# Kernel optimization log

Hardware: AMD Instinct MI355X
Metric: run time of the kernel (lower is better)

## Reference

```python
import jax, jax.numpy as jnp
import numpy as np

I, H, O = 3, 16, 5
B, S = 4096, 512


def setup_inputs() -> dict:
    key = jax.random.key(0)
    ks = jax.random.split(key, 4)
    scale = 0.1  # xavier gain=0.1 ballpark; exact init irrelevant for correctness baseline
    return {
        "x": jax.random.normal(ks[0], (B, S, I), dtype=jnp.float32),
        "W_ih": jax.random.normal(ks[1], (4 * H, I), dtype=jnp.float32) * scale,
        "W_hh": jax.random.normal(ks[2], (4 * H, H), dtype=jnp.float32) * scale,
        "b_ih": jnp.zeros((4 * H,), dtype=jnp.float32),
        "b_hh": jnp.zeros((4 * H,), dtype=jnp.float32),
        "W_lin": jax.random.normal(ks[3], (O, H), dtype=jnp.float32) * scale,
        "b_lin": jnp.zeros((O,), dtype=jnp.float32),
    }


def _lstm(x, W_ih, W_hh, b_ih, b_hh):
    # Precompute input contribution for all timesteps: [B, S, 4H]
    xg = jnp.einsum('bsi,gi->bsg', x, W_ih) + b_ih + b_hh
    xg = jnp.swapaxes(xg, 0, 1)  # [S, B, 4H] for scan
    h0 = jnp.zeros((x.shape[0], H), dtype=x.dtype)
    c0 = jnp.zeros_like(h0)

    def step(carry, xt):
        h, c = carry
        gates = xt + h @ W_hh.T  # [B, 4H]
        i, f, g, o = jnp.split(gates, 4, axis=-1)  # PyTorch gate order i,f,g,o
        i = jax.nn.sigmoid(i)
        f = jax.nn.sigmoid(f)
        g = jnp.tanh(g)
        o = jax.nn.sigmoid(o)
        c = f * c + i * g
        h = o * jnp.tanh(c)
        return (h, c), h

    _, hs = jax.lax.scan(step, (h0, c0), xg)
    return jnp.swapaxes(hs, 0, 1)  # [B, S, H]


def reference(x, W_ih, W_hh, b_ih, b_hh, W_lin, b_lin):
    out1 = _lstm(x, W_ih, W_hh, b_ih, b_hh)            # [B, S, H]
    out = jnp.einsum('bsh,oh->bso', out1, W_lin) + b_lin  # [B, S, O]
    return jnp.clip(out, -10.0, 10.0)
```

## Files before the change

kernel.cpp:

```cpp
#include <hip/hip_runtime.h>


#define TS 512
#define LOG2E 1.44269504088896340736f

typedef float f32x2 __attribute__((ext_vector_type(2)));

#define BCAST(K) hbr[K] = __int_as_float( \
    __builtin_amdgcn_update_dpp(0, hvi, 0x150 + (K), 0xf, 0xf, true))
#define BCAST8() \
  BCAST(0); BCAST(1); BCAST(2); BCAST(3); BCAST(4); BCAST(5); BCAST(6); BCAST(7)

static __device__ __forceinline__ float swz16(float v) {
  return __int_as_float(__builtin_amdgcn_ds_swizzle(__float_as_int(v), 0x401F));
}

__global__ __launch_bounds__(256)
__attribute__((amdgpu_waves_per_eu(2)))
void lstm_enc_kernel(const float* __restrict__ x,
                     const float* __restrict__ W_ih,
                     const float* __restrict__ W_hh,
                     const float* __restrict__ b_ih,
                     const float* __restrict__ b_hh,
                     const float* __restrict__ W_lin,
                     const float* __restrict__ b_lin,
                     float* __restrict__ out) {
  const int tid = threadIdx.x;
  const int u   = tid & 15;
  const int hh  = (tid >> 4) & 1;
  const int g8  = tid >> 5;
  const int l32 = tid & 31;
  const int batch = blockIdx.x * 8 + g8;
  const int jo = (u < 5) ? u : 0;

  __shared__ float4 xs[2][128][8];
  float4* xsf = &xs[0][0][0];

  f32x2 wif[8], wgo[8];
  float wl[8];
#pragma unroll
  for (int e = 0; e < 8; ++e) {
    const int k = hh * 8 + e;
    wif[e] = f32x2{W_hh[(u     ) * 16 + k] * LOG2E,
                   W_hh[(u + 16) * 16 + k] * LOG2E};
    wgo[e] = f32x2{W_hh[(u + 32) * 16 + k] * (2.0f * LOG2E),
                   W_hh[(u + 48) * 16 + k] * LOG2E};
    wl[e]  = W_lin[jo * 16 + k];
  }
  f32x2 xw[3], xwg[3];
#pragma unroll
  for (int i = 0; i < 3; ++i) {
    if (hh) {
      xw[i]  = f32x2{W_ih[(u     ) * 3 + i] * LOG2E,
                     W_ih[(u + 16) * 3 + i] * LOG2E};
      xwg[i] = f32x2{W_ih[(u + 32) * 3 + i] * (2.0f * LOG2E),
                     W_ih[(u + 48) * 3 + i] * LOG2E};
    } else {
      xw[i] = f32x2{0.f, 0.f};
      xwg[i] = f32x2{0.f, 0.f};
    }
  }
  const f32x2 bif = hh ? f32x2{0.f, 0.f}
                       : f32x2{(b_ih[u     ] + b_hh[u     ]) * LOG2E,
                               (b_ih[u + 16] + b_hh[u + 16]) * LOG2E};
  const f32x2 bgo = hh ? f32x2{0.f, 0.f}
                       : f32x2{(b_ih[u + 32] + b_hh[u + 32]) * (2.0f * LOG2E),
                               (b_ih[u + 48] + b_hh[u + 48]) * LOG2E};
  const float bl = hh ? 0.f : b_lin[jo];

  const float* __restrict__ xb = x + (size_t)batch * (TS * 3);
  float* __restrict__ ob = out + (size_t)batch * (TS * 5) + u;
  const bool storer = (u < 5) && (hh == 0);

  const float* xc0 = xb + l32 * 12;
  float4 q0, q1, q2;
  q0 = *(const float4*)(xc0 + 0);
  q1 = *(const float4*)(xc0 + 4);
  q2 = *(const float4*)(xc0 + 8);
  {
    const int wb = (l32 * 4) * 8 + g8;
    xsf[wb +  0] = float4{q0.x, q0.y, q0.z, 0.f};
    xsf[wb +  8] = float4{q0.w, q1.x, q1.y, 0.f};
    xsf[wb + 16] = float4{q1.z, q1.w, q2.x, 0.f};
    xsf[wb + 24] = float4{q2.y, q2.z, q2.w, 0.f};
  }
  q0 = *(const float4*)(xc0 + 384 + 0);
  q1 = *(const float4*)(xc0 + 384 + 4);
  q2 = *(const float4*)(xc0 + 384 + 8);

  float4 xr[2];
  xr[0] = xsf[0 * 8 + g8];
  xr[1] = xsf[1 * 8 + g8];

  float h = 0.0f, c = 0.0f;

  auto step = [&](int s, int slot) {
    const float4 xt = xr[slot];
    xr[slot] = xsf[(((s + 2) & 255) << 3) + g8];

    const float h_rot = __int_as_float(
        __builtin_amdgcn_update_dpp(0, __float_as_int(h), 0x128, 0xf, 0xf, true));
    const float hs = hh ? h_rot : h;
    const int hvi = __float_as_int(hs);
    float hbr[8];
    BCAST8();

    f32x2 aa = bif, ab = f32x2{0.f, 0.f};
    f32x2 ga = bgo, gb = f32x2{0.f, 0.f};
    float oa0 = bl, oa1 = 0.f;
    aa = f32x2{xt.x, xt.x} * xw[0] + aa;
    ab = f32x2{xt.y, xt.y} * xw[1] + ab;
    aa = f32x2{xt.z, xt.z} * xw[2] + aa;
    ga = f32x2{xt.x, xt.x} * xwg[0] + ga;
    gb = f32x2{xt.y, xt.y} * xwg[1] + gb;
    ga = f32x2{xt.z, xt.z} * xwg[2] + ga;
#pragma unroll
    for (int e = 0; e < 8; e += 2) {
      const f32x2 h0 = f32x2{hbr[e], hbr[e]};
      const f32x2 h1 = f32x2{hbr[e + 1], hbr[e + 1]};
      aa = h0 * wif[e] + aa;
      ab = h1 * wif[e + 1] + ab;
      ga = h0 * wgo[e] + ga;
      gb = h1 * wgo[e + 1] + gb;
      oa0 = fmaf(hbr[e], wl[e], oa0);
      oa1 = fmaf(hbr[e + 1], wl[e + 1], oa1);
    }
    const f32x2 zl = aa + ab;
    const f32x2 gl = ga + gb;
    const float oal = oa0 + oa1;

    const float zi  = zl.x + swz16(zl.x);
    const float zfg = zl.y + swz16(zl.y);
    const float zg  = gl.x + swz16(gl.x);
    const float zo  = gl.y + swz16(gl.y);
    const float oa  = oal + swz16(oal);

    if (s > 0 && storer) {
      ob[(s - 1) * 5] = fminf(fmaxf(oa, -10.0f), 10.0f);
    }

    const float ig = __builtin_amdgcn_rcpf(1.0f + __builtin_amdgcn_exp2f(-zi));
    const float fg = __builtin_amdgcn_rcpf(1.0f + __builtin_amdgcn_exp2f(-zfg));
    const float sg = __builtin_amdgcn_rcpf(1.0f + __builtin_amdgcn_exp2f(zg));
    const float og = __builtin_amdgcn_rcpf(1.0f + __builtin_amdgcn_exp2f(-zo));

    const float gg = fmaf(-2.0f, sg, 1.0f);
    c = fmaf(fg, c, ig * gg);
    const float tc = fmaf(-2.0f,
        __builtin_amdgcn_rcpf(1.0f + __builtin_amdgcn_exp2f((2.0f * LOG2E) * c)), 1.0f);
    h = og * tc;
  };

  for (int ch = 0; ch < 4; ++ch) {
    const int base = ch * 128;

#pragma unroll 2
    for (int v = 0; v < 64; ++v) step(base + v, v & 1);

    if (ch < 3) {
      const int p = (ch + 1) & 1;
      const int wb = (p * 128 + l32 * 4) * 8 + g8;
      xsf[wb +  0] = float4{q0.x, q0.y, q0.z, 0.f};
      xsf[wb +  8] = float4{q0.w, q1.x, q1.y, 0.f};
      xsf[wb + 16] = float4{q1.z, q1.w, q2.x, 0.f};
      xsf[wb + 24] = float4{q2.y, q2.z, q2.w, 0.f};
    }
    if (ch < 2) {
      const float* xc = xc0 + (ch + 2) * 384;
      q0 = *(const float4*)(xc + 0);
      q1 = *(const float4*)(xc + 4);
      q2 = *(const float4*)(xc + 8);
    }

#pragma unroll 2
    for (int v = 64; v < 128; ++v) step(base + v, v & 1);
  }

  {
    const float h_rot = __int_as_float(
        __builtin_amdgcn_update_dpp(0, __float_as_int(h), 0x128, 0xf, 0xf, true));
    const float hs = hh ? h_rot : h;
    const int hvi = __float_as_int(hs);
    float hbr[8];
    BCAST8();
    float oa0 = bl, oa1 = 0.f;
#pragma unroll
    for (int e = 0; e < 8; e += 2) {
      oa0 = fmaf(hbr[e], wl[e], oa0);
      oa1 = fmaf(hbr[e + 1], wl[e + 1], oa1);
    }
    const float oal = oa0 + oa1;
    const float oa = oal + swz16(oal);
    if (storer) {
      ob[(TS - 1) * 5] = fminf(fmaxf(oa, -10.0f), 10.0f);
    }
  }
}

extern "C" void kernel_launch(void* const* d_in, const int* in_sizes, int n_in,
                              void* d_out, int out_size, void* d_ws, size_t ws_size,
                              hipStream_t stream) {
  const float* x     = (const float*)d_in[0];
  const float* W_ih  = (const float*)d_in[1];
  const float* W_hh  = (const float*)d_in[2];
  const float* b_ih  = (const float*)d_in[3];
  const float* b_hh  = (const float*)d_in[4];
  const float* W_lin = (const float*)d_in[5];
  const float* b_lin = (const float*)d_in[6];
  float* out = (float*)d_out;

  const int B = in_sizes[0] / (TS * 3);
  const int grid = B / 8;
  lstm_enc_kernel<<<grid, 256, 0, stream>>>(x, W_ih, W_hh, b_ih, b_hh, W_lin, b_lin, out);
}
```

Baseline: 260.0 us.

## Split LSTM gates across half-waves instead of splitting the hidden dimension

Before, each 16-lane half computed partial sums over half of the recurrent inputs for all four gates and then reduced them across halves with swizzles. Now each half broadcasts all 16 hidden values and computes full dot products for two gates: input/forget in one half, cell/output in the other. The halves then exchange the activated gate values with only two swizzles. The two sigmoids in each lane share one reciprocal by computing rcp of the product of the two denominators, and the cell state is kept pre-scaled by 2*log2e to drop a multiply. The aim is fewer cross-lane ops and transcendental instructions on the serial per-step chain. The cost is more DPP broadcasts per step, and the shared reciprocal can overflow to inf and give NaN when both exponent terms are large.

Result: slower. 835.2 us (+221.3%).

```diff
diff --git a/kernel.cpp b/kernel.cpp
--- a/kernel.cpp
+++ b/kernel.cpp
@@ -8,8 +8,9 @@
 
 #define BCAST(K) hbr[K] = __int_as_float( \
     __builtin_amdgcn_update_dpp(0, hvi, 0x150 + (K), 0xf, 0xf, true))
-#define BCAST8() \
-  BCAST(0); BCAST(1); BCAST(2); BCAST(3); BCAST(4); BCAST(5); BCAST(6); BCAST(7)
+#define BCAST_ALL() \
+  BCAST(0); BCAST(1); BCAST(2); BCAST(3); BCAST(4); BCAST(5); BCAST(6); BCAST(7); \
+  BCAST(8); BCAST(9); BCAST(10); BCAST(11); BCAST(12); BCAST(13); BCAST(14); BCAST(15)
 
 static __device__ __forceinline__ float swz16(float v) {
   return __int_as_float(__builtin_amdgcn_ds_swizzle(__float_as_int(v), 0x401F));
@@ -29,49 +30,39 @@
   const int u   = tid & 15;
   const int hh  = (tid >> 4) & 1;
   const int g8  = tid >> 5;
-  const int l32 = tid & 31;
   const int batch = blockIdx.x * 8 + g8;
   const int jo = (u < 5) ? u : 0;
 
   __shared__ float4 xs[2][128][8];
   float4* xsf = &xs[0][0][0];
 
-  f32x2 wif[8], wgo[8];
+  const int r0 = u + (hh ? 32 : 0);
+  const int r1 = u + (hh ? 48 : 16);
+  const float s0 = hh ? (-2.0f * LOG2E) : LOG2E;
+  const float s1 = LOG2E;
+
+  f32x2 wp[16];
   float wl[8];
 #pragma unroll
-  for (int e = 0; e < 8; ++e) {
-    const int k = hh * 8 + e;
-    wif[e] = f32x2{W_hh[(u     ) * 16 + k] * LOG2E,
-                   W_hh[(u + 16) * 16 + k] * LOG2E};
-    wgo[e] = f32x2{W_hh[(u + 32) * 16 + k] * (2.0f * LOG2E),
-                   W_hh[(u + 48) * 16 + k] * LOG2E};
-    wl[e]  = W_lin[jo * 16 + k];
-  }
-  f32x2 xw[3], xwg[3];
+  for (int k = 0; k < 16; ++k) {
+    wp[k] = f32x2{W_hh[r0 * 16 + k] * s0, W_hh[r1 * 16 + k] * s1};
+  }
+#pragma unroll
+  for (int e = 0; e < 8; ++e) wl[e] = W_lin[jo * 16 + hh * 8 + e];
+  f32x2 xwp[3];
 #pragma unroll
   for (int i = 0; i < 3; ++i) {
-    if (hh) {
-      xw[i]  = f32x2{W_ih[(u     ) * 3 + i] * LOG2E,
-                     W_ih[(u + 16) * 3 + i] * LOG2E};
-      xwg[i] = f32x2{W_ih[(u + 32) * 3 + i] * (2.0f * LOG2E),
-                     W_ih[(u + 48) * 3 + i] * LOG2E};
-    } else {
-      xw[i] = f32x2{0.f, 0.f};
-      xwg[i] = f32x2{0.f, 0.f};
-    }
-  }
-  const f32x2 bif = hh ? f32x2{0.f, 0.f}
-                       : f32x2{(b_ih[u     ] + b_hh[u     ]) * LOG2E,
-                               (b_ih[u + 16] + b_hh[u + 16]) * LOG2E};
-  const f32x2 bgo = hh ? f32x2{0.f, 0.f}
-                       : f32x2{(b_ih[u + 32] + b_hh[u + 32]) * (2.0f * LOG2E),
-                               (b_ih[u + 48] + b_hh[u + 48]) * LOG2E};
+    xwp[i] = f32x2{W_ih[r0 * 3 + i] * s0, W_ih[r1 * 3 + i] * s1};
+  }
+  const f32x2 bp = f32x2{(b_ih[r0] + b_hh[r0]) * s0,
+                         (b_ih[r1] + b_hh[r1]) * s1};
   const float bl = hh ? 0.f : b_lin[jo];
 
   const float* __restrict__ xb = x + (size_t)batch * (TS * 3);
   float* __restrict__ ob = out + (size_t)batch * (TS * 5) + u;
   const bool storer = (u < 5) && (hh == 0);
 
+  const int l32 = tid & 31;
   const float* xc0 = xb + l32 * 12;
   float4 q0, q1, q2;
   q0 = *(const float4*)(xc0 + 0);
@@ -92,62 +83,63 @@
   xr[0] = xsf[0 * 8 + g8];
   xr[1] = xsf[1 * 8 + g8];
 
-  float h = 0.0f, c = 0.0f;
+  float h = 0.0f, cs = 0.0f;
 
   auto step = [&](int s, int slot) {
     const float4 xt = xr[slot];
     xr[slot] = xsf[(((s + 2) & 255) << 3) + g8];
 
-    const float h_rot = __int_as_float(
-        __builtin_amdgcn_update_dpp(0, __float_as_int(h), 0x128, 0xf, 0xf, true));
-    const float hs = hh ? h_rot : h;
-    const int hvi = __float_as_int(hs);
-    float hbr[8];
-    BCAST8();
-
-    f32x2 aa = bif, ab = f32x2{0.f, 0.f};
-    f32x2 ga = bgo, gb = f32x2{0.f, 0.f};
+    float hbr[16];
+    const int hvi = __float_as_int(h);
+    BCAST_ALL();
+
+    f32x2 aa = bp, ab = f32x2{0.f, 0.f}, ac = f32x2{0.f, 0.f}, ad = f32x2{0.f, 0.f};
     float oa0 = bl, oa1 = 0.f;
-    aa = f32x2{xt.x, xt.x} * xw[0] + aa;
-    ab = f32x2{xt.y, xt.y} * xw[1] + ab;
-    aa = f32x2{xt.z, xt.z} * xw[2] + aa;
-    ga = f32x2{xt.x, xt.x} * xwg[0] + ga;
-    gb = f32x2{xt.y, xt.y} * xwg[1] + gb;
-    ga = f32x2{xt.z, xt.z} * xwg[2] + ga;
+    aa = f32x2{xt.x, xt.x} * xwp[0] + aa;
+    ab = f32x2{xt.y, xt.y} * xwp[1] + ab;
+    ac = f32x2{xt.z, xt.z} * xwp[2] + ac;
+#pragma unroll
+    for (int k = 0; k < 16; k += 4) {
+      const f32x2 h0 = f32x2{hbr[k],     hbr[k]};
+      const f32x2 h1 = f32x2{hbr[k + 1], hbr[k + 1]};
+      const f32x2 h2 = f32x2{hbr[k + 2], hbr[k + 2]};
+      const f32x2 h3 = f32x2{hbr[k + 3], hbr[k + 3]};
+      aa = h0 * wp[k]     + aa;
+      ab = h1 * wp[k + 1] + ab;
+      ac = h2 * wp[k + 2] + ac;
+      ad = h3 * wp[k + 3] + ad;
+    }
 #pragma unroll
     for (int e = 0; e < 8; e += 2) {
-      const f32x2 h0 = f32x2{hbr[e], hbr[e]};
-      const f32x2 h1 = f32x2{hbr[e + 1], hbr[e + 1]};
-      aa = h0 * wif[e] + aa;
-      ab = h1 * wif[e + 1] + ab;
-      ga = h0 * wgo[e] + ga;
-      gb = h1 * wgo[e + 1] + gb;
-      oa0 = fmaf(hbr[e], wl[e], oa0);
-      oa1 = fmaf(hbr[e + 1], wl[e + 1], oa1);
-    }
-    const f32x2 zl = aa + ab;
-    const f32x2 gl = ga + gb;
+      oa0 = fmaf(hbr[hh * 8 + e],     wl[e],     oa0);
+      oa1 = fmaf(hbr[hh * 8 + e + 1], wl[e + 1], oa1);
+    }
+    const f32x2 z = (aa + ab) + (ac + ad);
+
     const float oal = oa0 + oa1;
-
-    const float zi  = zl.x + swz16(zl.x);
-    const float zfg = zl.y + swz16(zl.y);
-    const float zg  = gl.x + swz16(gl.x);
-    const float zo  = gl.y + swz16(gl.y);
-    const float oa  = oal + swz16(oal);
-
+    const float oa = oal + swz16(oal);
     if (s > 0 && storer) {
       ob[(s - 1) * 5] = fminf(fmaxf(oa, -10.0f), 10.0f);
     }
 
-    const float ig = __builtin_amdgcn_rcpf(1.0f + __builtin_amdgcn_exp2f(-zi));
-    const float fg = __builtin_amdgcn_rcpf(1.0f + __builtin_amdgcn_exp2f(-zfg));
-    const float sg = __builtin_amdgcn_rcpf(1.0f + __builtin_amdgcn_exp2f(zg));
-    const float og = __builtin_amdgcn_rcpf(1.0f + __builtin_amdgcn_exp2f(-zo));
-
-    const float gg = fmaf(-2.0f, sg, 1.0f);
-    c = fmaf(fg, c, ig * gg);
+    const float E0 = __builtin_amdgcn_exp2f(-z.x);
+    const float E1 = __builtin_amdgcn_exp2f(-z.y);
+    const float d0 = 1.0f + E0, d1 = 1.0f + E1;
+    const float R  = __builtin_amdgcn_rcpf(d0 * d1);
+    const float v0 = d1 * R;
+    const float v1 = d0 * R;
+
+    const float w0 = swz16(v0);
+    const float w1 = swz16(v1);
+    const float ig = hh ? w0 : v0;
+    const float fg = hh ? w1 : v1;
+    const float sg = hh ? v0 : w0;
+    const float og = hh ? v1 : w1;
+
+    const float gg2 = fmaf(-4.0f * LOG2E, sg, 2.0f * LOG2E);
+    cs = fmaf(fg, cs, ig * gg2);
     const float tc = fmaf(-2.0f,
-        __builtin_amdgcn_rcpf(1.0f + __builtin_amdgcn_exp2f((2.0f * LOG2E) * c)), 1.0f);
+        __builtin_amdgcn_rcpf(1.0f + __builtin_amdgcn_exp2f(cs)), 1.0f);
     h = og * tc;
   };
 
@@ -177,17 +169,14 @@
   }
 
   {
-    const float h_rot = __int_as_float(
-        __builtin_amdgcn_update_dpp(0, __float_as_int(h), 0x128, 0xf, 0xf, true));
-    const float hs = hh ? h_rot : h;
-    const int hvi = __float_as_int(hs);
-    float hbr[8];
-    BCAST8();
+    float hbr[16];
+    const int hvi = __float_as_int(h);
+    BCAST_ALL();
     float oa0 = bl, oa1 = 0.f;
 #pragma unroll
     for (int e = 0; e < 8; e += 2) {
-      oa0 = fmaf(hbr[e], wl[e], oa0);
-      oa1 = fmaf(hbr[e + 1], wl[e + 1], oa1);
+      oa0 = fmaf(hbr[hh * 8 + e],     wl[e],     oa0);
+      oa1 = fmaf(hbr[hh * 8 + e + 1], wl[e + 1], oa1);
     }
     const float oal = oa0 + oa1;
     const float oa = oal + swz16(oal);
```
